# Optimization experiments

Measured on AMD Instinct MI355X. Metric: run time of the kernel, lower is better.

The kernel has to match this reference:

```python
import jax, jax.numpy as jnp
import numpy as np


def setup_inputs() -> dict:
    key = jax.random.key(0)
    ks = jax.random.split(key, 9)
    B, C, H, W = 16, 512, 64, 64
    s = 1.0 / np.sqrt(C)  # fan-in style init scale for 1x1 conv weights
    x = jax.random.normal(ks[0], (B, C, H, W), dtype=jnp.float32)
    W_theta = jax.random.normal(ks[1], (C, C), dtype=jnp.float32) * s
    b_theta = jax.random.normal(ks[2], (C,), dtype=jnp.float32) * 0.01
    W_phi = jax.random.normal(ks[3], (C, C), dtype=jnp.float32) * s
    b_phi = jax.random.normal(ks[4], (C,), dtype=jnp.float32) * 0.01
    W_g = jax.random.normal(ks[5], (C, C), dtype=jnp.float32) * s
    b_g = jax.random.normal(ks[6], (C,), dtype=jnp.float32) * 0.01
    W_out = jax.random.normal(ks[7], (C, C), dtype=jnp.float32) * s
    b_out = jax.random.normal(ks[8], (C,), dtype=jnp.float32) * 0.01
    return {
        "x": x,
        "W_theta": W_theta, "b_theta": b_theta,
        "W_phi": W_phi, "b_phi": b_phi,
        "W_g": W_g, "b_g": b_g,
        "W_out": W_out, "b_out": b_out,
    }


def reference(x, W_theta, b_theta, W_phi, b_phi, W_g, b_g, W_out, b_out):
    B, C, H, W = x.shape
    n = H * W
    xf = x.reshape(B, C, n)  # [B, C, HW]

    def conv1x1(Wm, b):
        # 1x1 conv == channel-mixing GEMM: [O,C] x [B,C,N] -> [B,O,N]
        return jnp.einsum('oc,bcn->bon', Wm, xf) + b[None, :, None]

    phi = conv1x1(W_phi, b_phi)      # [B, C, HW]
    theta = conv1x1(W_theta, b_theta)  # [B, C, HW] (used transposed: 'b (h w) c')
    g = conv1x1(W_g, b_g)            # [B, C, HW]

    # phi @ theta^T over spatial dim -> [B, C, C] channel-channel attention
    scores = jnp.einsum('bcn,bdn->bcd', phi, theta) * (1.0 / C)
    attn = jax.nn.softmax(scores, axis=2)  # softmax over last (dim=2), as in torch
    Y = jnp.einsum('bcd,bdn->bcn', attn, g)  # [B, C, HW]

    A = jnp.einsum('oc,bcn->bon', W_out, Y) + b_out[None, :, None]
    return x + A.reshape(B, C, H, W)
```

## Files before the change

### kernel.cpp

```cpp
#include <hip/hip_runtime.h>
#include <hip/hip_bf16.h>
#include <stdint.h>


typedef unsigned short u16;
typedef __attribute__((ext_vector_type(8))) short frag8;
typedef __attribute__((ext_vector_type(4))) float f32x4;

__device__ __forceinline__ u16 f2bf(float f) {
  union { __hip_bfloat16 h; u16 u; } c; c.h = __float2bfloat16(f); return c.u;
}

__device__ __forceinline__ void gl_lds16(const u16* g, u16* l) {
  __builtin_amdgcn_global_load_lds(
      (const __attribute__((address_space(1))) void*)g,
      (__attribute__((address_space(3))) void*)l, 16, 0, 0);
}

#define SCHED0 __builtin_amdgcn_sched_barrier(0)
#define SBAR   __builtin_amdgcn_s_barrier()

__global__ __launch_bounds__(256) void prep_x(const float* __restrict__ X,
                                              u16* __restrict__ XT,
                                              u16* __restrict__ XB,
                                              float* __restrict__ S) {
  const int b = blockIdx.z;
  const int n0 = blockIdx.x * 64;
  const int c0 = blockIdx.y * 64;
  __shared__ u16 t[64][72];
  const float* Xb = X + (int64_t)b * (512LL * 4096);
  const int tid = threadIdx.x;
  const int r = tid >> 3;
  const int e8 = (tid & 7) * 8;
#pragma unroll
  for (int p = 0; p < 2; p++) {
    const int row = p * 32 + r;
    const int c = c0 + row;
    const float4 f0 = *(const float4*)(Xb + (int64_t)c * 4096 + n0 + e8);
    const float4 f1 = *(const float4*)(Xb + (int64_t)c * 4096 + n0 + e8 + 4);
    union { uint4 q; u16 u[8]; } pk;
    pk.u[0] = f2bf(f0.x); pk.u[1] = f2bf(f0.y); pk.u[2] = f2bf(f0.z); pk.u[3] = f2bf(f0.w);
    pk.u[4] = f2bf(f1.x); pk.u[5] = f2bf(f1.y); pk.u[6] = f2bf(f1.z); pk.u[7] = f2bf(f1.w);
    *(uint4*)(XB + ((int64_t)b * 512 + c) * 4096 + n0 + e8) = pk.q;
    *(uint4*)&t[row][e8 ^ (row & 56)] = pk.q;
    float s = f0.x + f0.y + f0.z + f0.w + f1.x + f1.y + f1.z + f1.w;
    s += __shfl_xor(s, 1); s += __shfl_xor(s, 2); s += __shfl_xor(s, 4);
    if ((tid & 7) == 0) atomicAdd(&S[b * 512 + c], s);
  }
  __syncthreads();
#pragma unroll
  for (int p = 0; p < 2; p++) {
    const int nr = p * 32 + r;
    union { uint4 q; u16 u[8]; } o;
#pragma unroll
    for (int j = 0; j < 8; j++)
      o.u[j] = t[e8 + j][nr ^ e8];
    *(uint4*)(XT + ((int64_t)b * 4096 + n0 + nr) * 512 + c0 + e8) = o.q;
  }
}

__constant__ const int g_ty[10] = {0,0,0,0,1,1,1,2,2,3};
__constant__ const int g_tx[10] = {0,1,2,3,1,2,3,2,3,3};

__global__ __launch_bounds__(256) void gram_sk(const u16* __restrict__ XB,
                                               u16* __restrict__ G) {
  const int b = blockIdx.z;
  const int tl = blockIdx.x;
  const int m0 = g_ty[tl] * 128, n0 = g_tx[tl] * 128;
  const int tid = threadIdx.x;
  const int lane = tid & 63, wave = tid >> 6;
  __shared__ u16 sA[3][4096];
  __shared__ u16 sB[3][4096];
  const u16* Xb = XB + (int64_t)b * (512LL * 4096);

  f32x4 acc[4][4];
#pragma unroll
  for (int i = 0; i < 4; i++)
#pragma unroll
    for (int j = 0; j < 4; j++)
#pragma unroll
      for (int r = 0; r < 4; r++) acc[i][j][r] = 0.0f;

  const int fr = lane & 15;
  const int fkx = (((lane >> 4) ^ ((fr >> 1) & 3))) * 8;
  const int wm = (wave & 1) * 64, wn = (wave >> 1) * 64;

  const int srow = tid >> 2;
  const int scol = (((tid & 3) ^ ((tid >> 3) & 3))) * 8;
  const u16* Ar0 = Xb + (int64_t)(m0 + srow) * 4096 + scol;
  const u16* Ar1 = Xb + (int64_t)(m0 + 64 + srow) * 4096 + scol;
  const u16* Br0 = Xb + (int64_t)(n0 + srow) * 4096 + scol;
  const u16* Br1 = Xb + (int64_t)(n0 + 64 + srow) * 4096 + scol;

  auto stage = [&](int t, int buf) {
    gl_lds16(Ar0 + t * 32, sA[buf] + tid * 8);
    gl_lds16(Ar1 + t * 32, sA[buf] + 2048 + tid * 8);
    gl_lds16(Br0 + t * 32, sB[buf] + tid * 8);
    gl_lds16(Br1 + t * 32, sB[buf] + 2048 + tid * 8);
  };
  auto comp = [&](int buf) {
    frag8 af[4], bf[4];
#pragma unroll
    for (int i = 0; i < 4; i++) {
      af[i] = *(const frag8*)(sA[buf] + (wm + i * 16 + fr) * 32 + fkx);
      bf[i] = *(const frag8*)(sB[buf] + (wn + i * 16 + fr) * 32 + fkx);
    }
#pragma unroll
    for (int i = 0; i < 4; i++)
#pragma unroll
      for (int j = 0; j < 4; j++)
        acc[i][j] = __builtin_amdgcn_mfma_f32_16x16x32_bf16(af[i], bf[j], acc[i][j], 0, 0, 0);
  };

  stage(0, 0); stage(1, 1);
  for (int t = 0; t < 126; t++) {
    SCHED0; SBAR; SCHED0;
    stage(t + 2, (t + 2) % 3);
    asm volatile("s_waitcnt vmcnt(8)" ::: "memory");
    SBAR; SCHED0;
    comp(t % 3);
  }
  asm volatile("s_waitcnt vmcnt(0)" ::: "memory");
  SBAR; SCHED0;
  comp(0);
  comp(1);

  u16* Gb = G + (int64_t)b * 262144;
  const int quad = lane >> 4;
#pragma unroll
  for (int i = 0; i < 4; i++)
#pragma unroll
    for (int j = 0; j < 4; j++) {
      const int row0 = m0 + wm + i * 16 + quad * 4;
      const int col = n0 + wn + j * 16 + fr;
      union { u16 u[4]; uint2 v; } mg;
#pragma unroll
      for (int r = 0; r < 4; r++) {
        const u16 h = f2bf(acc[i][j][r]);
        Gb[(int64_t)(row0 + r) * 512 + col] = h;
        mg.u[r] = h;
      }
      if (m0 != n0)
        *(uint2*)(Gb + (int64_t)col * 512 + row0) = mg.v;
    }
}

enum { EPI_BF16 = 0, EPI_SCORES = 1, EPI_BF16I = 2 };

template <int EPI>
__global__ __launch_bounds__(256) void gemm128_bt(
    const u16* __restrict__ A, int64_t sAb, int lda,
    const u16* __restrict__ B, int64_t sBb, int ldb,
    void* __restrict__ Cv, int64_t sCb, int ldc,
    const float* __restrict__ e_bphi, const float* __restrict__ e_btheta,
    const float* __restrict__ e_uphi, const float* __restrict__ e_utheta) {
  const int b = blockIdx.z;
  const int m0 = blockIdx.y * 128, n0 = blockIdx.x * 128;
  const int tid = threadIdx.x;
  const int lane = tid & 63, wave = tid >> 6;
  __shared__ u16 sA[4][4096];
  __shared__ u16 sB[4][4096];
  const u16* Ab = A + (int64_t)b * sAb;
  const u16* Bb = B + (int64_t)b * sBb;

  f32x4 acc[4][4];
#pragma unroll
  for (int i = 0; i < 4; i++)
#pragma unroll
    for (int j = 0; j < 4; j++)
#pragma unroll
      for (int r = 0; r < 4; r++) acc[i][j][r] = 0.0f;

  const int srow = tid >> 2;
  const int scol = (((tid & 3) ^ ((tid >> 3) & 3))) * 8;
  const int fr = lane & 15;
  const int fkx = (((lane >> 4) ^ ((fr >> 1) & 3))) * 8;
  const int wm = (wave & 1) * 64, wn = (wave >> 1) * 64;

  const u16* Ar0 = Ab + (int64_t)(m0 + srow) * lda + scol;
  const u16* Ar1 = Ab + (int64_t)(m0 + 64 + srow) * lda + scol;
  const u16* Br0 = Bb + (int64_t)(n0 + srow) * ldb + scol;
  const u16* Br1 = Bb + (int64_t)(n0 + 64 + srow) * ldb + scol;

  auto stage = [&](int t, int buf) {
    gl_lds16(Ar0 + t * 32, sA[buf] + tid * 8);
    gl_lds16(Ar1 + t * 32, sA[buf] + 2048 + tid * 8);
    gl_lds16(Br0 + t * 32, sB[buf] + tid * 8);
    gl_lds16(Br1 + t * 32, sB[buf] + 2048 + tid * 8);
  };
  auto comp = [&](int buf) {
    frag8 af[4], bf[4];
#pragma unroll
    for (int i = 0; i < 4; i++) {
      af[i] = *(const frag8*)(sA[buf] + (wm + i * 16 + fr) * 32 + fkx);
      bf[i] = *(const frag8*)(sB[buf] + (wn + i * 16 + fr) * 32 + fkx);
    }
#pragma unroll
    for (int i = 0; i < 4; i++)
#pragma unroll
      for (int j = 0; j < 4; j++)
        acc[i][j] = __builtin_amdgcn_mfma_f32_16x16x32_bf16(af[i], bf[j], acc[i][j], 0, 0, 0);
  };

  stage(0, 0); stage(1, 1); stage(2, 2);
#pragma unroll
  for (int t = 0; t < 13; t++) {
    SCHED0; SBAR; SCHED0;
    stage(t + 3, (t + 3) % 4);
    asm volatile("s_waitcnt vmcnt(12)" ::: "memory");
    SBAR; SCHED0;
    comp(t % 4);
  }
  asm volatile("s_waitcnt vmcnt(8)" ::: "memory");
  SBAR; SCHED0;
  comp(13 % 4);
  asm volatile("s_waitcnt vmcnt(4)" ::: "memory");
  SBAR; SCHED0;
  comp(14 % 4);
  asm volatile("s_waitcnt vmcnt(0)" ::: "memory");
  SBAR; SCHED0;
  comp(15 % 4);

  const int quad = lane >> 4;
#pragma unroll
  for (int i = 0; i < 4; i++)
#pragma unroll
    for (int j = 0; j < 4; j++)
#pragma unroll
      for (int r = 0; r < 4; r++) {
        const int row = m0 + wm + i * 16 + quad * 4 + r;
        const int col = n0 + wn + j * 16 + fr;
        const float a = acc[i][j][r];
        if constexpr (EPI == EPI_BF16) {
          ((u16*)Cv)[(int64_t)b * sCb + (int64_t)row * ldc + col] = f2bf(a);
        } else if constexpr (EPI == EPI_BF16I) {
          ((u16*)Cv)[(int64_t)b * sCb + (int64_t)row * ldc + col] =
              f2bf(a + (row == col ? 1.0f : 0.0f));
        } else {
          const float bp = e_bphi[row];
          const float bt = e_btheta[col];
          ((float*)Cv)[(int64_t)b * sCb + (int64_t)row * ldc + col] =
              (a + bp * e_utheta[b * 512 + col] + bt * e_uphi[b * 512 + row] +
               4096.0f * bp * bt) * (1.0f / 512.0f);
        }
      }
}

__global__ __launch_bounds__(256) void gemm_final(const u16* __restrict__ M,
                                                  const u16* __restrict__ XT,
                                                  const float* __restrict__ V,
                                                  float* __restrict__ O) {
  const int b = blockIdx.z;
  const int m0 = blockIdx.y * 128, n0 = blockIdx.x * 128;
  const int tid = threadIdx.x;
  const int lane = tid & 63, wave = tid >> 6;
  __shared__ u16 sA[2][4096];
  __shared__ u16 sB[2][4096];
  const u16* Ab = M + (int64_t)b * 262144;
  const u16* Bb = XT + (int64_t)b * (4096LL * 512);

  f32x4 acc[4][4];
#pragma unroll
  for (int i = 0; i < 4; i++)
#pragma unroll
    for (int j = 0; j < 4; j++)
#pragma unroll
      for (int r = 0; r < 4; r++) acc[i][j][r] = 0.0f;

  const int srow = tid >> 2;
  const int scol = (((tid & 3) ^ ((tid >> 3) & 3))) * 8;
  const int fr = lane & 15;
  const int fkx = (((lane >> 4) ^ ((fr >> 1) & 3))) * 8;
  const int wm = (wave & 1) * 64, wn = (wave >> 1) * 64;

  const u16* Ar0 = Ab + (int64_t)(m0 + srow) * 512 + scol;
  const u16* Ar1 = Ab + (int64_t)(m0 + 64 + srow) * 512 + scol;
  const u16* Br0 = Bb + (int64_t)(n0 + srow) * 512 + scol;
  const u16* Br1 = Bb + (int64_t)(n0 + 64 + srow) * 512 + scol;

  gl_lds16(Ar0, sA[0] + tid * 8);
  gl_lds16(Ar1, sA[0] + 2048 + tid * 8);
  gl_lds16(Br0, sB[0] + tid * 8);
  gl_lds16(Br1, sB[0] + 2048 + tid * 8);
  __syncthreads();

  for (int k0 = 0; k0 < 512; k0 += 32) {
    const int cur = (k0 >> 5) & 1;
    if (k0 + 32 < 512) {
      u16* dA = sA[cur ^ 1];
      u16* dB = sB[cur ^ 1];
      gl_lds16(Ar0 + k0 + 32, dA + tid * 8);
      gl_lds16(Ar1 + k0 + 32, dA + 2048 + tid * 8);
      gl_lds16(Br0 + k0 + 32, dB + tid * 8);
      gl_lds16(Br1 + k0 + 32, dB + 2048 + tid * 8);
    }
    frag8 af[4], bf[4];
#pragma unroll
    for (int i = 0; i < 4; i++) {
      af[i] = *(const frag8*)(sA[cur] + (wm + i * 16 + fr) * 32 + fkx);
      bf[i] = *(const frag8*)(sB[cur] + (wn + i * 16 + fr) * 32 + fkx);
    }
#pragma unroll
    for (int i = 0; i < 4; i++)
#pragma unroll
      for (int j = 0; j < 4; j++)
        acc[i][j] = __builtin_amdgcn_mfma_f32_16x16x32_bf16(af[i], bf[j], acc[i][j], 0, 0, 0);
    __syncthreads();
  }

  const int quad = lane >> 4;
#pragma unroll
  for (int i = 0; i < 4; i++)
#pragma unroll
    for (int j = 0; j < 4; j++)
#pragma unroll
      for (int r = 0; r < 4; r++) {
        const int row = m0 + wm + i * 16 + quad * 4 + r;
        const int col = n0 + wn + j * 16 + fr;
        O[(int64_t)b * (512LL * 4096) + (int64_t)row * 4096 + col] =
            acc[i][j][r] + V[b * 512 + row];
      }
}

__global__ __launch_bounds__(256) void uv_kernel(const float* __restrict__ Wphi,
                                                 const float* __restrict__ Wtheta,
                                                 const float* __restrict__ S,
                                                 float* __restrict__ UPH, float* __restrict__ UTH) {
  const int b = blockIdx.x;
  const int o0 = blockIdx.y * 64;
  const int tid = threadIdx.x;
  __shared__ float s[512];
  s[tid] = S[b * 512 + tid];
  s[tid + 256] = S[b * 512 + tid + 256];
  __syncthreads();
  const int o = o0 + (tid >> 2);
  const int q = tid & 3;
  float a0 = 0.f, a1 = 0.f;
  for (int c = q * 128; c < q * 128 + 128; c += 4) {
    const float4 wa = *(const float4*)(Wphi + (int64_t)o * 512 + c);
    const float4 wb = *(const float4*)(Wtheta + (int64_t)o * 512 + c);
    a0 += wa.x * s[c] + wa.y * s[c + 1] + wa.z * s[c + 2] + wa.w * s[c + 3];
    a1 += wb.x * s[c] + wb.y * s[c + 1] + wb.z * s[c + 2] + wb.w * s[c + 3];
  }
  a0 += __shfl_xor(a0, 1); a0 += __shfl_xor(a0, 2);
  a1 += __shfl_xor(a1, 1); a1 += __shfl_xor(a1, 2);
  if (q == 0) {
    UPH[b * 512 + o] = a0;
    UTH[b * 512 + o] = a1;
  }
}

__global__ __launch_bounds__(256) void v_kernel(const float* __restrict__ Wout,
                                                const float* __restrict__ R,
                                                const float* __restrict__ bout,
                                                float* __restrict__ V) {
  const int b = blockIdx.x;
  const int o0 = blockIdx.y * 64;
  const int tid = threadIdx.x;
  __shared__ float s[512];
  s[tid] = R[b * 512 + tid];
  s[tid + 256] = R[b * 512 + tid + 256];
  __syncthreads();
  const int o = o0 + (tid >> 2);
  const int q = tid & 3;
  float a0 = 0.f;
  for (int c = q * 128; c < q * 128 + 128; c += 4) {
    const float4 wa = *(const float4*)(Wout + (int64_t)o * 512 + c);
    a0 += wa.x * s[c] + wa.y * s[c + 1] + wa.z * s[c + 2] + wa.w * s[c + 3];
  }
  a0 += __shfl_xor(a0, 1); a0 += __shfl_xor(a0, 2);
  if (q == 0) V[b * 512 + o] = a0 + bout[o];
}

__global__ __launch_bounds__(256) void convert_w(const float* __restrict__ W0,
                                                 const float* __restrict__ W1,
                                                 const float* __restrict__ W2,
                                                 u16* __restrict__ O0, u16* __restrict__ O1,
                                                 u16* __restrict__ O2) {
  const int idx = blockIdx.x * 256 + threadIdx.x;
  const int m = idx >> 16;
  const int off = (idx & 65535) * 4;
  const float* src = (m == 0) ? W0 : (m == 1) ? W1 : W2;
  u16* dst = (m == 0) ? O0 : (m == 1) ? O1 : O2;
  const float4 f = *(const float4*)(src + off);
  union { u16 u[4]; uint2 v; } p;
  p.u[0] = f2bf(f.x); p.u[1] = f2bf(f.y); p.u[2] = f2bf(f.z); p.u[3] = f2bf(f.w);
  *(uint2*)(dst + off) = p.v;
}

__global__ void wg_transpose(const float* __restrict__ Wg, u16* __restrict__ WgT) {
  __shared__ float t[16][17];
  const int i0 = blockIdx.y * 16, j0 = blockIdx.x * 16;
  t[threadIdx.y][threadIdx.x] = Wg[(i0 + threadIdx.y) * 512 + j0 + threadIdx.x];
  __syncthreads();
  WgT[(j0 + threadIdx.y) * 512 + i0 + threadIdx.x] = f2bf(t[threadIdx.x][threadIdx.y]);
}

__global__ __launch_bounds__(64) void softmax_k(float* __restrict__ SC,
                                                const float* __restrict__ bg,
                                                float* __restrict__ R) {
  const int row = blockIdx.x;
  const int lane = threadIdx.x;
  float* Sr = SC + (int64_t)row * 512;
  union { float4 q[2]; float v[8]; } u;
  u.q[0] = *(const float4*)(Sr + lane * 8);
  u.q[1] = *(const float4*)(Sr + lane * 8 + 4);
  const float4 g0 = *(const float4*)(bg + lane * 8);
  const float4 g1 = *(const float4*)(bg + lane * 8 + 4);
  const float gb[8] = { g0.x, g0.y, g0.z, g0.w, g1.x, g1.y, g1.z, g1.w };
  float m = u.v[0];
#pragma unroll
  for (int j = 1; j < 8; j++) m = fmaxf(m, u.v[j]);
#pragma unroll
  for (int off = 32; off > 0; off >>= 1) m = fmaxf(m, __shfl_xor(m, off));
  float e[8], s = 0.f, sb = 0.f;
#pragma unroll
  for (int j = 0; j < 8; j++) {
    e[j] = __expf(u.v[j] - m);
    s += e[j];
    sb += e[j] * gb[j];
  }
#pragma unroll
  for (int off = 32; off > 0; off >>= 1) { s += __shfl_xor(s, off); sb += __shfl_xor(sb, off); }
  const float inv = 1.0f / s;
  union { uint4 q; u16 h[8]; } o;
#pragma unroll
  for (int j = 0; j < 8; j++) o.h[j] = f2bf(e[j] * inv);
  *(uint4*)((u16*)SC + (int64_t)row * 1024 + lane * 8) = o.q;
  if (lane == 0) R[row] = sb * inv;
}

extern "C" void kernel_launch(void* const* d_in, const int* in_sizes, int n_in,
                              void* d_out, int out_size, void* d_ws, size_t ws_size,
                              hipStream_t stream) {
  const float* x      = (const float*)d_in[0];
  const float* Wtheta = (const float*)d_in[1];
  const float* btheta = (const float*)d_in[2];
  const float* Wphi   = (const float*)d_in[3];
  const float* bphi   = (const float*)d_in[4];
  const float* Wg     = (const float*)d_in[5];
  const float* bg     = (const float*)d_in[6];
  const float* Wout   = (const float*)d_in[7];
  const float* bout   = (const float*)d_in[8];

  char* ws = (char*)d_ws;
  u16*   xT     = (u16*)(ws + 0);
  u16*   G      = (u16*)(ws + 67108864);
  u16*   T1     = (u16*)(ws + 75497472);
  float* SC     = (float*)(ws + 83886080);
  u16*   Wphib  = (u16*)(ws + 100663296);
  u16*   Wthetab= (u16*)(ws + 101187584);
  u16*   Woutb  = (u16*)(ws + 101711872);
  u16*   WgTb   = (u16*)(ws + 102236160);
  float* S      = (float*)(ws + 102760448);
  float* UPH    = (float*)(ws + 102793216);
  float* UTH    = (float*)(ws + 102825984);
  float* R      = (float*)(ws + 102858752);
  float* V      = (float*)(ws + 102891520);
  u16* ATT = (u16*)SC;
  u16* Q = G;
  u16* M = T1;

  u16*   XB = (u16*)d_out;

  hipMemsetAsync(S, 0, 32768, stream);
  prep_x<<<dim3(64, 8, 16), 256, 0, stream>>>(x, xT, XB, S);
  uv_kernel<<<dim3(16, 8), 256, 0, stream>>>(Wphi, Wtheta, S, UPH, UTH);
  convert_w<<<768, 256, 0, stream>>>(Wphi, Wtheta, Wout, Wphib, Wthetab, Woutb);
  wg_transpose<<<dim3(32, 32), dim3(16, 16), 0, stream>>>(Wg, WgTb);
  gram_sk<<<dim3(10, 1, 16), 256, 0, stream>>>(XB, G);
  gemm128_bt<EPI_BF16><<<dim3(4, 4, 16), 256, 0, stream>>>(
      Wphib, 0, 512, G, 512LL * 512, 512, T1, 512LL * 512, 512,
      nullptr, nullptr, nullptr, nullptr);
  gemm128_bt<EPI_SCORES><<<dim3(4, 4, 16), 256, 0, stream>>>(
      T1, 512LL * 512, 512, Wthetab, 0, 512, SC, 512LL * 512, 512,
      bphi, btheta, UPH, UTH);
  softmax_k<<<8192, 64, 0, stream>>>(SC, bg, R);
  gemm128_bt<EPI_BF16><<<dim3(4, 4, 16), 256, 0, stream>>>(
      WgTb, 0, 512, ATT, 512LL * 1024, 1024, Q, 512LL * 512, 512,
      nullptr, nullptr, nullptr, nullptr);
  gemm128_bt<EPI_BF16I><<<dim3(4, 4, 16), 256, 0, stream>>>(
      Woutb, 0, 512, Q, 512LL * 512, 512, M, 512LL * 512, 512,
      nullptr, nullptr, nullptr, nullptr);
  v_kernel<<<dim3(16, 8), 256, 0, stream>>>(Wout, R, bout, V);
  gemm_final<<<dim3(32, 4, 16), 256, 0, stream>>>(M, xT, V, (float*)d_out);
}
```

Measured before the change: 453.6 us.

## Double gram kernel K-tile to 64 and remap blocks for XCD locality

```diff
diff --git a/kernel.cpp b/kernel.cpp
--- a/kernel.cpp
+++ b/kernel.cpp
@@ -64,13 +64,15 @@
 
 __global__ __launch_bounds__(256) void gram_sk(const u16* __restrict__ XB,
                                                u16* __restrict__ G) {
-  const int b = blockIdx.z;
-  const int tl = blockIdx.x;
+  const int flat = blockIdx.x;
+  const int w = (flat & 7) * 20 + (flat >> 3);
+  const int b = w / 10;
+  const int tl = w - b * 10;
   const int m0 = g_ty[tl] * 128, n0 = g_tx[tl] * 128;
   const int tid = threadIdx.x;
   const int lane = tid & 63, wave = tid >> 6;
-  __shared__ u16 sA[3][4096];
-  __shared__ u16 sB[3][4096];
+  __shared__ u16 sA[3][8192];
+  __shared__ u16 sB[3][8192];
   const u16* Xb = XB + (int64_t)b * (512LL * 4096);
 
   f32x4 acc[4][4];
@@ -82,48 +84,54 @@
       for (int r = 0; r < 4; r++) acc[i][j][r] = 0.0f;
 
   const int fr = lane & 15;
-  const int fkx = (((lane >> 4) ^ ((fr >> 1) & 3))) * 8;
+  const int hi = lane >> 4;
+  const int fkx0 = ((hi) ^ (fr & 7)) * 8;
+  const int fkx1 = ((4 + hi) ^ (fr & 7)) * 8;
   const int wm = (wave & 1) * 64, wn = (wave >> 1) * 64;
 
-  const int srow = tid >> 2;
-  const int scol = (((tid & 3) ^ ((tid >> 3) & 3))) * 8;
-  const u16* Ar0 = Xb + (int64_t)(m0 + srow) * 4096 + scol;
-  const u16* Ar1 = Xb + (int64_t)(m0 + 64 + srow) * 4096 + scol;
-  const u16* Br0 = Xb + (int64_t)(n0 + srow) * 4096 + scol;
-  const u16* Br1 = Xb + (int64_t)(n0 + 64 + srow) * 4096 + scol;
+  const int srow = tid >> 3;
+  const int scol = (((tid & 7) ^ ((tid >> 3) & 7))) * 8;
+  const u16* ArA = Xb + (int64_t)(m0 + srow) * 4096 + scol;
+  const u16* BrA = Xb + (int64_t)(n0 + srow) * 4096 + scol;
 
   auto stage = [&](int t, int buf) {
-    gl_lds16(Ar0 + t * 32, sA[buf] + tid * 8);
-    gl_lds16(Ar1 + t * 32, sA[buf] + 2048 + tid * 8);
-    gl_lds16(Br0 + t * 32, sB[buf] + tid * 8);
-    gl_lds16(Br1 + t * 32, sB[buf] + 2048 + tid * 8);
+    const u16* a = ArA + t * 64;
+    const u16* bb = BrA + t * 64;
+#pragma unroll
+    for (int d = 0; d < 4; d++) {
+      gl_lds16(a + (int64_t)d * (32 * 4096), sA[buf] + d * 2048 + tid * 8);
+      gl_lds16(bb + (int64_t)d * (32 * 4096), sB[buf] + d * 2048 + tid * 8);
+    }
   };
   auto comp = [&](int buf) {
-    frag8 af[4], bf[4];
-#pragma unroll
-    for (int i = 0; i < 4; i++) {
-      af[i] = *(const frag8*)(sA[buf] + (wm + i * 16 + fr) * 32 + fkx);
-      bf[i] = *(const frag8*)(sB[buf] + (wn + i * 16 + fr) * 32 + fkx);
-    }
-#pragma unroll
-    for (int i = 0; i < 4; i++)
-#pragma unroll
-      for (int j = 0; j < 4; j++)
-        acc[i][j] = __builtin_amdgcn_mfma_f32_16x16x32_bf16(af[i], bf[j], acc[i][j], 0, 0, 0);
+#pragma unroll
+    for (int kk = 0; kk < 2; kk++) {
+      const int fx = kk ? fkx1 : fkx0;
+      frag8 af[4], bf[4];
+#pragma unroll
+      for (int i = 0; i < 4; i++) {
+        af[i] = *(const frag8*)(sA[buf] + (wm + i * 16 + fr) * 64 + fx);
+        bf[i] = *(const frag8*)(sB[buf] + (wn + i * 16 + fr) * 64 + fx);
+      }
+#pragma unroll
+      for (int i = 0; i < 4; i++)
+#pragma unroll
+        for (int j = 0; j < 4; j++)
+          acc[i][j] = __builtin_amdgcn_mfma_f32_16x16x32_bf16(af[i], bf[j], acc[i][j], 0, 0, 0);
+    }
   };
 
   stage(0, 0); stage(1, 1);
-  for (int t = 0; t < 126; t++) {
+  for (int t = 0; t < 62; t++) {
     SCHED0; SBAR; SCHED0;
     stage(t + 2, (t + 2) % 3);
-    asm volatile("s_waitcnt vmcnt(8)" ::: "memory");
+    asm volatile("s_waitcnt vmcnt(16)" ::: "memory");
     SBAR; SCHED0;
     comp(t % 3);
   }
   asm volatile("s_waitcnt vmcnt(0)" ::: "memory");
   SBAR; SCHED0;
-  comp(0);
-  comp(1);
+  comp(62 % 3); comp(63 % 3);
 
   u16* Gb = G + (int64_t)b * 262144;
   const int quad = lane >> 4;
@@ -468,7 +476,7 @@
   uv_kernel<<<dim3(16, 8), 256, 0, stream>>>(Wphi, Wtheta, S, UPH, UTH);
   convert_w<<<768, 256, 0, stream>>>(Wphi, Wtheta, Wout, Wphib, Wthetab, Woutb);
   wg_transpose<<<dim3(32, 32), dim3(16, 16), 0, stream>>>(Wg, WgTb);
-  gram_sk<<<dim3(10, 1, 16), 256, 0, stream>>>(XB, G);
+  gram_sk<<<dim3(160), 256, 0, stream>>>(XB, G);
   gemm128_bt<EPI_BF16><<<dim3(4, 4, 16), 256, 0, stream>>>(
       Wphib, 0, 512, G, 512LL * 512, 512, T1, 512LL * 512, 512,
       nullptr, nullptr, nullptr, nullptr);
```

New measurement: 463.2 us. +2.1%, slower.
